# Kernel tuning notes

Measured on AMD Instinct MI355X. Metric: run time of the kernel, lower is better.

The kernel has to match this reference:

```python
import jax, jax.numpy as jnp
import numpy as np

IN_F = 4096
OUT_F = 4096
Q_RANK = 2
R_RANK = 2
SCALE = 1.0
B, S = 2, 2048


def setup_inputs() -> dict:
    key = jax.random.key(0)
    ks = jax.random.split(key, 8)
    inp = jax.random.normal(ks[0], (B, S, IN_F), jnp.float32)
    # Q, R come from a QR decomposition of linear.weight.t(); random stand-ins with
    # matching shapes and O(1) scale are fine for a numerical baseline.
    Q = jax.random.normal(ks[1], (IN_F, OUT_F), jnp.float32) / np.sqrt(IN_F).astype(np.float32)
    R = jax.random.normal(ks[2], (OUT_F, OUT_F), jnp.float32) / np.sqrt(OUT_F).astype(np.float32)
    # kron_Q1/Q2 are initialized to identity in __init__ (never re-initialized);
    # add small noise so the rotation path is non-trivial.
    sq1 = IN_F // Q_RANK
    kron_Q1 = jnp.eye(sq1, dtype=jnp.float32) + 0.01 * jax.random.normal(ks[3], (sq1, sq1), jnp.float32)
    kron_Q2 = jnp.eye(Q_RANK, dtype=jnp.float32) + 0.01 * jax.random.normal(ks[4], (Q_RANK, Q_RANK), jnp.float32)
    # kron_R1/R2 use normal init with std = 1/size.
    sr1 = OUT_F // R_RANK
    kron_R1 = jax.random.normal(ks[5], (sr1, sr1), jnp.float32) / sr1
    kron_R2 = jax.random.normal(ks[6], (R_RANK, R_RANK), jnp.float32) / R_RANK
    # lambda_matrix inits to zeros; use small noise so the delta term is exercised.
    lambda_matrix = 0.01 * jax.random.normal(ks[7], (OUT_F,), jnp.float32)
    return {"input": inp, "Q": Q, "R": R, "kron_Q1": kron_Q1, "kron_Q2": kron_Q2,
            "kron_R1": kron_R1, "kron_R2": kron_R2, "lambda_matrix": lambda_matrix}


def reference(input, Q, R, kron_Q1, kron_Q2, kron_R1, kron_R2, lambda_matrix):
    rotation = jnp.kron(kron_Q1, kron_Q2)          # [in, in]
    orth = jnp.kron(kron_R1, kron_R2)              # [out, out]
    # orth @ diag(lambda) @ orth.T without materializing diag
    R_eff = R + (orth * lambda_matrix[None, :]) @ orth.T  # [out, out]
    W_t = rotation @ (Q @ R_eff)                   # [in, out]
    # F.linear(input, W_t.t()) == input @ W_t; dropout is identity in eval; bias=False
    return (input @ W_t) * SCALE
```

## Files before the change

### kernel.cpp

```cpp
#include <hip/hip_runtime.h>
#include <stdint.h>


typedef unsigned short u16;
typedef short bf16x8 __attribute__((ext_vector_type(8)));
typedef float f32x16 __attribute__((ext_vector_type(16)));

__device__ __forceinline__ u16 f2bf(float f) {
  union { float f; uint32_t u; } v; v.f = f;
  return (u16)((v.u + 0x7FFFu + ((v.u >> 16) & 1u)) >> 16);
}

__device__ __forceinline__ void store_out(float* p, float v) { *p = v; }
__device__ __forceinline__ void store_out(u16* p, float v) { *p = f2bf(v); }

__device__ __forceinline__ void gload_lds16(const u16* g, u16* l) {
  __builtin_amdgcn_global_load_lds(
      (__attribute__((address_space(1))) void*)(uintptr_t)g,
      (__attribute__((address_space(3))) void*)l, 16, 0, 0);
}

#define MFMA32(a, b, c) __builtin_amdgcn_mfma_f32_32x32x16_bf16((a), (b), (c), 0, 0, 0)

template <typename OutT>
__global__ __launch_bounds__(512, 2) void gemm256(
    const u16* __restrict__ A, const u16* __restrict__ Bt, OutT* __restrict__ C,
    int M, int N, int K, int ldC, long long sA, long long sC) {
  extern __shared__ __align__(16) u16 smem[];
  u16* ldsA = smem;
  u16* ldsB = smem + 32768;

  const int tid  = (int)threadIdx.x;
  const int lane = tid & 63;
  const int wid  = tid >> 6;
  const int wr   = wid >> 2;
  const int wc   = wid & 3;

  const int tilesX = (int)gridDim.x;
  const int tilesXY = tilesX * (int)gridDim.y;
  const int nwg = tilesXY * (int)gridDim.z;
  const int bid = ((int)blockIdx.z * (int)gridDim.y + (int)blockIdx.y) * tilesX + (int)blockIdx.x;
  const int swz = (bid & 7) * (nwg >> 3) + (bid >> 3);
  const int z   = swz / tilesXY;
  const int rem = swz % tilesXY;
  const int brow = (rem / tilesX) << 8;
  const int bcol = (rem % tilesX) << 8;
  A += (size_t)z * sA;
  C += (size_t)z * sC;

  const int hh  = (lane & 15) >> 1;
  const int gq  = lane >> 4;
  const int par = lane & 1;
  const int sfr = (((gq + 4 * par) ^ hh) << 3) + (hh << 6);
  const int abase = wr * 4096 + sfr;
  const int bbase = (wc >> 1) * 4096 + (wc & 1) * 2048 + sfr;

  {
  }
  const int Rw  = (wid << 3) + (lane >> 3);
  const int hS  = Rw & 7;
  const int xS  = (lane & 7) ^ hS;
  const int srow = ((Rw >> 4) << 5) + ((xS & 1) << 4) + (hS << 1) + (xS >> 2);
  const int scol = (((Rw >> 3) & 1) << 4) + (((xS >> 1) & 1) << 3);
  const size_t gA0 = (size_t)(brow + srow) * K + scol;
  const size_t gB0 = (size_t)(bcol + srow) * K + scol;
  const size_t rstep = (size_t)K << 7;
  const int sdst = wid * 512;

  const int NC = K >> 5;

  f32x16 acc[4][2] = {};
  bf16x8 af[2][2], bf[2][2];

#define STG_A(c, rh) gload_lds16(A + gA0 + (rh) * rstep + (size_t)(c) * 32, \
    ldsA + ((c) & 3) * 8192 + (rh) * 4096 + sdst)
#define STG_B(c, rh) gload_lds16(Bt + gB0 + (rh) * rstep + (size_t)(c) * 32, \
    ldsB + ((c) & 3) * 8192 + (rh) * 4096 + sdst)
#define VM8 asm volatile("s_waitcnt vmcnt(8)" ::: "memory")
#define VM4 asm volatile("s_waitcnt vmcnt(4)" ::: "memory")
#define VM0 asm volatile("s_waitcnt vmcnt(0)" ::: "memory")
#define NOPW (void)0

#define P_EVEN(bb, S, W) do {                                                   \
    const u16* _pa = ldsA + (bb) * 8192 + abase;                                \
    const u16* _pb = ldsB + (bb) * 8192 + bbase;                                \
    af[0][0] = *(const bf16x8*)(_pa);                                           \
    af[0][1] = *(const bf16x8*)(_pa + 512);                                     \
    af[1][0] = *(const bf16x8*)(_pa + 1024);                                    \
    af[1][1] = *(const bf16x8*)(_pa + 1536);                                    \
    bf[0][0] = *(const bf16x8*)(_pb);                                           \
    bf[0][1] = *(const bf16x8*)(_pb + 512);                                     \
    bf[1][0] = *(const bf16x8*)(_pb + 1024);                                    \
    bf[1][1] = *(const bf16x8*)(_pb + 1536);                                    \
    S;                                                                          \
    __builtin_amdgcn_s_barrier();                                               \
    __builtin_amdgcn_s_setprio(1);                                              \
    acc[0][0] = MFMA32(af[0][0], bf[0][0], acc[0][0]);                          \
    acc[0][0] = MFMA32(af[0][1], bf[0][1], acc[0][0]);                          \
    acc[0][1] = MFMA32(af[0][0], bf[1][0], acc[0][1]);                          \
    acc[0][1] = MFMA32(af[0][1], bf[1][1], acc[0][1]);                          \
    acc[1][0] = MFMA32(af[1][0], bf[0][0], acc[1][0]);                          \
    acc[1][0] = MFMA32(af[1][1], bf[0][1], acc[1][0]);                          \
    acc[1][1] = MFMA32(af[1][0], bf[1][0], acc[1][1]);                          \
    acc[1][1] = MFMA32(af[1][1], bf[1][1], acc[1][1]);                          \
    __builtin_amdgcn_s_setprio(0);                                              \
    W;                                                                          \
    __builtin_amdgcn_s_barrier();                                               \
  } while (0)

#define P_ODD(bb, S, W) do {                                                    \
    const u16* _pa = ldsA + (bb) * 8192 + abase;                                \
    af[0][0] = *(const bf16x8*)(_pa + 2048);                                    \
    af[0][1] = *(const bf16x8*)(_pa + 2560);                                    \
    af[1][0] = *(const bf16x8*)(_pa + 3072);                                    \
    af[1][1] = *(const bf16x8*)(_pa + 3584);                                    \
    S;                                                                          \
    __builtin_amdgcn_s_barrier();                                               \
    __builtin_amdgcn_s_setprio(1);                                              \
    acc[2][0] = MFMA32(af[0][0], bf[0][0], acc[2][0]);                          \
    acc[2][0] = MFMA32(af[0][1], bf[0][1], acc[2][0]);                          \
    acc[2][1] = MFMA32(af[0][0], bf[1][0], acc[2][1]);                          \
    acc[2][1] = MFMA32(af[0][1], bf[1][1], acc[2][1]);                          \
    acc[3][0] = MFMA32(af[1][0], bf[0][0], acc[3][0]);                          \
    acc[3][0] = MFMA32(af[1][1], bf[0][1], acc[3][0]);                          \
    acc[3][1] = MFMA32(af[1][0], bf[1][0], acc[3][1]);                          \
    acc[3][1] = MFMA32(af[1][1], bf[1][1], acc[3][1]);                          \
    __builtin_amdgcn_s_setprio(0);                                              \
    W;                                                                          \
    __builtin_amdgcn_s_barrier();                                               \
  } while (0)

#define ITER(bb, c, DO3, DO4, W1, W3) do {                                      \
    P_EVEN((bb),     if (DO3) { STG_A((c) + 3, 0); STG_A((c) + 3, 1); }, NOPW); \
    P_ODD ((bb),     if (DO3) { STG_B((c) + 3, 0); STG_B((c) + 3, 1); }, W1);   \
    P_EVEN((bb) + 1, if (DO4) { STG_A((c) + 4, 0); STG_A((c) + 4, 1); }, NOPW); \
    P_ODD ((bb) + 1, if (DO4) { STG_B((c) + 4, 0); STG_B((c) + 4, 1); }, W3);   \
  } while (0)

  STG_A(0, 0); STG_A(0, 1); STG_B(0, 0); STG_B(0, 1);
  STG_A(1, 0); STG_A(1, 1); STG_B(1, 0); STG_B(1, 1);
  STG_A(2, 0); STG_A(2, 1); STG_B(2, 0); STG_B(2, 1);
  VM8;
  __builtin_amdgcn_s_barrier();

  for (int c = 0; c + 4 < NC; c += 4) {
    ITER(0, c,     1, 1, VM8, VM8);
    ITER(2, c + 2, 1, 1, VM8, VM8);
  }
  ITER(0, NC - 4, 1, 0, VM8, VM4);
  ITER(2, NC - 2, 0, 0, VM0, NOPW);

#undef ITER
#undef P_EVEN
#undef P_ODD
#undef STG_A
#undef STG_B
#undef VM8
#undef VM4
#undef VM0
#undef NOPW

  const int l31 = lane & 31;
  const int lg2 = lane >> 5;
#pragma unroll
  for (int m = 0; m < 4; ++m) {
    const int rb = brow + wr * 128 + m * 32 + 4 * lg2;
#pragma unroll
    for (int n = 0; n < 2; ++n) {
      const int cc = bcol + wc * 64 + n * 32 + l31;
#pragma unroll
      for (int q = 0; q < 4; ++q)
#pragma unroll
        for (int j = 0; j < 4; ++j)
          store_out(&C[(size_t)(rb + 8 * q + j) * ldC + cc], acc[m][n][q * 4 + j]);
    }
  }
}

__global__ void trans_kernel(const float* __restrict__ in, u16* __restrict__ out, int n) {
  __shared__ float t[32][33];
  const int bx = (int)blockIdx.x * 32, by = (int)blockIdx.y * 32;
  const int x = (int)threadIdx.x, y0 = (int)threadIdx.y;
#pragma unroll
  for (int dy = 0; dy < 32; dy += 8)
    t[y0 + dy][x] = in[(size_t)(bx + y0 + dy) * n + by + x];
  __syncthreads();
#pragma unroll
  for (int dy = 0; dy < 32; dy += 8)
    out[(size_t)(by + y0 + dy) * n + bx + x] = f2bf(t[x][y0 + dy]);
}

__global__ void transperm_kernel(const float* __restrict__ in, u16* __restrict__ out) {
  __shared__ float t[32][33];
  const int bx = (int)blockIdx.x * 32, by = (int)blockIdx.y * 32;
  const int x = (int)threadIdx.x, y0 = (int)threadIdx.y;
#pragma unroll
  for (int dy = 0; dy < 32; dy += 8)
    t[y0 + dy][x] = in[(size_t)(bx + y0 + dy) * 4096 + by + x];
  __syncthreads();
  const int r = bx + x;
  const int cp = ((r & 1) << 11) | (r >> 1);
#pragma unroll
  for (int dy = 0; dy < 32; dy += 8)
    out[(size_t)(by + y0 + dy) * 4096 + cp] = f2bf(t[x][y0 + dy]);
}

__global__ void transadd_kernel(const float* __restrict__ R, const float* __restrict__ Dsub,
                                u16* __restrict__ out) {
  __shared__ float t[32][33];
  const int bx = (int)blockIdx.x * 32, by = (int)blockIdx.y * 32;
  const int x = (int)threadIdx.x, y0 = (int)threadIdx.y;
#pragma unroll
  for (int dy = 0; dy < 32; dy += 8)
    t[y0 + dy][x] = R[(size_t)(bx + y0 + dy) * 4096 + by + x];
  __syncthreads();
  const int j = bx + x;
#pragma unroll
  for (int dy = 0; dy < 32; dy += 8) {
    const int i = by + y0 + dy;
    const int s = ((i & 1) << 1) | (j & 1);
    const float d = Dsub[(size_t)s * 4194304 + ((size_t)(i >> 1) << 11) + (j >> 1)];
    out[(size_t)i * 4096 + j] = f2bf(t[x][y0 + dy] + d);
  }
}

__global__ void scale_r1_kernel(const float* __restrict__ R1, const float* __restrict__ R2,
                                const float* __restrict__ lam,
                                u16* __restrict__ R1bf, u16* __restrict__ Asc) {
  const int idx = (int)blockIdx.x * 256 + (int)threadIdx.x;
  const int i1 = idx >> 9, k1 = (idx & 511) << 2;
  const float4 r1 = *(const float4*)(R1 + (size_t)i1 * 2048 + k1);
  const float4 l0 = *(const float4*)(lam + 2 * k1);
  const float4 l1 = *(const float4*)(lam + 2 * k1 + 4);
  const float le[4] = {l0.x, l0.z, l1.x, l1.z};
  const float lo[4] = {l0.y, l0.w, l1.y, l1.w};
  const float rv[4] = {r1.x, r1.y, r1.z, r1.w};
  ushort4 rb;
  rb.x = f2bf(r1.x); rb.y = f2bf(r1.y); rb.z = f2bf(r1.z); rb.w = f2bf(r1.w);
  *(ushort4*)(R1bf + (size_t)i1 * 2048 + k1) = rb;
#pragma unroll
  for (int s = 0; s < 4; ++s) {
    const int i2 = s >> 1, j2 = s & 1;
    const float c0 = R2[i2 * 2] * R2[j2 * 2];
    const float c1 = R2[i2 * 2 + 1] * R2[j2 * 2 + 1];
    ushort4 o;
    u16* dst = Asc + (size_t)s * 4194304 + (size_t)i1 * 2048 + k1;
    o.x = f2bf(rv[0] * (le[0] * c0 + lo[0] * c1));
    o.y = f2bf(rv[1] * (le[1] * c0 + lo[1] * c1));
    o.z = f2bf(rv[2] * (le[2] * c0 + lo[2] * c1));
    o.w = f2bf(rv[3] * (le[3] * c0 + lo[3] * c1));
    *(ushort4*)dst = o;
  }
}

__global__ void tprep_kernel(const float* __restrict__ in, const float* __restrict__ Q2,
                             u16* __restrict__ T) {
  const int idx = (int)blockIdx.x * 256 + (int)threadIdx.x;
  const int s = idx >> 9, k1 = (idx & 511) << 2;
  const float4 a = *(const float4*)(in + (size_t)s * 4096 + 2 * k1);
  const float4 b = *(const float4*)(in + (size_t)s * 4096 + 2 * k1 + 4);
  const float e[4] = {a.x, a.z, b.x, b.z};
  const float o[4] = {a.y, a.w, b.y, b.w};
  const float q00 = Q2[0], q01 = Q2[1], q10 = Q2[2], q11 = Q2[3];
  ushort4 t0, t1;
  t0.x = f2bf(e[0] * q00 + o[0] * q10); t1.x = f2bf(e[0] * q01 + o[0] * q11);
  t0.y = f2bf(e[1] * q00 + o[1] * q10); t1.y = f2bf(e[1] * q01 + o[1] * q11);
  t0.z = f2bf(e[2] * q00 + o[2] * q10); t1.z = f2bf(e[2] * q01 + o[2] * q11);
  t0.w = f2bf(e[3] * q00 + o[3] * q10); t1.w = f2bf(e[3] * q01 + o[3] * q11);
  *(ushort4*)(T + (size_t)s * 2048 + k1) = t0;
  *(ushort4*)(T + 8388608 + (size_t)s * 2048 + k1) = t1;
}

extern "C" void kernel_launch(void* const* d_in, const int* in_sizes, int n_in,
                              void* d_out, int out_size, void* d_ws, size_t ws_size,
                              hipStream_t stream) {
  const float* input = (const float*)d_in[0];
  const float* Q     = (const float*)d_in[1];
  const float* R     = (const float*)d_in[2];
  const float* Q1    = (const float*)d_in[3];
  const float* Q2    = (const float*)d_in[4];
  const float* R1    = (const float*)d_in[5];
  const float* R2    = (const float*)d_in[6];
  const float* lam   = (const float*)d_in[7];
  float* out = (float*)d_out;

  const size_t MB = 1024ull * 1024ull;
  char* ws = (char*)d_ws;
  u16* R1bf  = (u16*)(ws + 0 * MB);
  u16* Asc   = (u16*)(ws + 8 * MB);
  u16* Q1tb  = (u16*)(ws + 40 * MB);
  u16* T     = (u16*)(ws + 48 * MB);
  u16* Qtp   = (u16*)(ws + 80 * MB);
  u16* rteff = (u16*)(ws + 112 * MB);
  u16* X1p   = (u16*)(ws + 144 * MB);
  u16* X2    = Asc;
  float* Dsub = (float*)d_out;

  {
    void (*pf)(const u16*, const u16*, float*, int, int, int, int, long long, long long) = gemm256<float>;
    void (*pb)(const u16*, const u16*, u16*, int, int, int, int, long long, long long)   = gemm256<u16>;
    (void)hipFuncSetAttribute((const void*)pf, hipFuncAttributeMaxDynamicSharedMemorySize, 131072);
    (void)hipFuncSetAttribute((const void*)pb, hipFuncAttributeMaxDynamicSharedMemorySize, 131072);
  }

  const dim3 tb(32, 8);
  trans_kernel<<<dim3(64, 64), tb, 0, stream>>>(Q1, Q1tb, 2048);
  transperm_kernel<<<dim3(128, 128), tb, 0, stream>>>(Q, Qtp);
  scale_r1_kernel<<<4096, 256, 0, stream>>>(R1, R2, lam, R1bf, Asc);
  tprep_kernel<<<8192, 256, 0, stream>>>(input, Q2, T);
  gemm256<float><<<dim3(8, 8, 4), 512, 131072, stream>>>(
      Asc, R1bf, Dsub, 2048, 2048, 2048, 2048, 4194304LL, 4194304LL);
  transadd_kernel<<<dim3(128, 128), tb, 0, stream>>>(R, Dsub, rteff);
  gemm256<u16><<<dim3(8, 16, 2), 512, 131072, stream>>>(
      T, Q1tb, X1p, 4096, 2048, 2048, 4096, 8388608LL, 2048LL);
  gemm256<u16><<<dim3(16, 16, 1), 512, 131072, stream>>>(
      X1p, Qtp, X2, 4096, 4096, 4096, 4096, 0LL, 0LL);
  gemm256<float><<<dim3(16, 16, 1), 512, 131072, stream>>>(
      X2, rteff, out, 4096, 4096, 4096, 4096, 0LL, 0LL);
}
```

Baseline: 507.5 us.

## Merge even/odd half-phases into one phase per K-chunk with full-stage prefetch

Replaces the two half-phases per K-chunk (A rows 0-1, then rows 2-3, each with its own barrier pair) with a single phase. Each phase loads all four A fragments plus the B fragments, issues 16 MFMAs, and prefetches a whole stage (A and B) three chunks ahead. This halves the number of barriers and waitcnt points per chunk and gives longer MFMA runs between synchronisations. In exchange it needs more VGPRs for the extra A fragments, which may lower occupancy. It also reworks the vmcnt accounting, and the tail of the loop has to drain the prefetched stages correctly.

Result: slower. 549.2 us (+8.2%).

```diff
diff --git a/kernel.cpp b/kernel.cpp
--- a/kernel.cpp
+++ b/kernel.cpp
@@ -55,8 +55,6 @@
   const int abase = wr * 4096 + sfr;
   const int bbase = (wc >> 1) * 4096 + (wc & 1) * 2048 + sfr;
 
-  {
-  }
   const int Rw  = (wid << 3) + (lane >> 3);
   const int hS  = Rw & 7;
   const int xS  = (lane & 7) ^ hS;
@@ -70,28 +68,34 @@
   const int NC = K >> 5;
 
   f32x16 acc[4][2] = {};
-  bf16x8 af[2][2], bf[2][2];
+  bf16x8 af[4][2], bf[2][2];
 
 #define STG_A(c, rh) gload_lds16(A + gA0 + (rh) * rstep + (size_t)(c) * 32, \
     ldsA + ((c) & 3) * 8192 + (rh) * 4096 + sdst)
 #define STG_B(c, rh) gload_lds16(Bt + gB0 + (rh) * rstep + (size_t)(c) * 32, \
     ldsB + ((c) & 3) * 8192 + (rh) * 4096 + sdst)
+#define STAGE(c) do { STG_A(c, 0); STG_A(c, 1); STG_B(c, 0); STG_B(c, 1); } while (0)
 #define VM8 asm volatile("s_waitcnt vmcnt(8)" ::: "memory")
 #define VM4 asm volatile("s_waitcnt vmcnt(4)" ::: "memory")
 #define VM0 asm volatile("s_waitcnt vmcnt(0)" ::: "memory")
 #define NOPW (void)0
 
-#define P_EVEN(bb, S, W) do {                                                   \
+#define PH(bb, S, W) do {                                                       \
+    __builtin_amdgcn_sched_barrier(0);                                          \
     const u16* _pa = ldsA + (bb) * 8192 + abase;                                \
     const u16* _pb = ldsB + (bb) * 8192 + bbase;                                \
+    bf[0][0] = *(const bf16x8*)(_pb);                                           \
+    bf[0][1] = *(const bf16x8*)(_pb + 512);                                     \
+    bf[1][0] = *(const bf16x8*)(_pb + 1024);                                    \
+    bf[1][1] = *(const bf16x8*)(_pb + 1536);                                    \
     af[0][0] = *(const bf16x8*)(_pa);                                           \
     af[0][1] = *(const bf16x8*)(_pa + 512);                                     \
     af[1][0] = *(const bf16x8*)(_pa + 1024);                                    \
     af[1][1] = *(const bf16x8*)(_pa + 1536);                                    \
-    bf[0][0] = *(const bf16x8*)(_pb);                                           \
-    bf[0][1] = *(const bf16x8*)(_pb + 512);                                     \
-    bf[1][0] = *(const bf16x8*)(_pb + 1024);                                    \
-    bf[1][1] = *(const bf16x8*)(_pb + 1536);                                    \
+    af[2][0] = *(const bf16x8*)(_pa + 2048);                                    \
+    af[2][1] = *(const bf16x8*)(_pa + 2560);                                    \
+    af[3][0] = *(const bf16x8*)(_pa + 3072);                                    \
+    af[3][1] = *(const bf16x8*)(_pa + 3584);                                    \
     S;                                                                          \
     __builtin_amdgcn_s_barrier();                                               \
     __builtin_amdgcn_s_setprio(1);                                              \
@@ -103,56 +107,36 @@
     acc[1][0] = MFMA32(af[1][1], bf[0][1], acc[1][0]);                          \
     acc[1][1] = MFMA32(af[1][0], bf[1][0], acc[1][1]);                          \
     acc[1][1] = MFMA32(af[1][1], bf[1][1], acc[1][1]);                          \
+    acc[2][0] = MFMA32(af[2][0], bf[0][0], acc[2][0]);                          \
+    acc[2][0] = MFMA32(af[2][1], bf[0][1], acc[2][0]);                          \
+    acc[2][1] = MFMA32(af[2][0], bf[1][0], acc[2][1]);                          \
+    acc[2][1] = MFMA32(af[2][1], bf[1][1], acc[2][1]);                          \
+    acc[3][0] = MFMA32(af[3][0], bf[0][0], acc[3][0]);                          \
+    acc[3][0] = MFMA32(af[3][1], bf[0][1], acc[3][0]);                          \
+    acc[3][1] = MFMA32(af[3][0], bf[1][0], acc[3][1]);                          \
+    acc[3][1] = MFMA32(af[3][1], bf[1][1], acc[3][1]);                          \
     __builtin_amdgcn_s_setprio(0);                                              \
     W;                                                                          \
     __builtin_amdgcn_s_barrier();                                               \
   } while (0)
 
-#define P_ODD(bb, S, W) do {                                                    \
-    const u16* _pa = ldsA + (bb) * 8192 + abase;                                \
-    af[0][0] = *(const bf16x8*)(_pa + 2048);                                    \
-    af[0][1] = *(const bf16x8*)(_pa + 2560);                                    \
-    af[1][0] = *(const bf16x8*)(_pa + 3072);                                    \
-    af[1][1] = *(const bf16x8*)(_pa + 3584);                                    \
-    S;                                                                          \
-    __builtin_amdgcn_s_barrier();                                               \
-    __builtin_amdgcn_s_setprio(1);                                              \
-    acc[2][0] = MFMA32(af[0][0], bf[0][0], acc[2][0]);                          \
-    acc[2][0] = MFMA32(af[0][1], bf[0][1], acc[2][0]);                          \
-    acc[2][1] = MFMA32(af[0][0], bf[1][0], acc[2][1]);                          \
-    acc[2][1] = MFMA32(af[0][1], bf[1][1], acc[2][1]);                          \
-    acc[3][0] = MFMA32(af[1][0], bf[0][0], acc[3][0]);                          \
-    acc[3][0] = MFMA32(af[1][1], bf[0][1], acc[3][0]);                          \
-    acc[3][1] = MFMA32(af[1][0], bf[1][0], acc[3][1]);                          \
-    acc[3][1] = MFMA32(af[1][1], bf[1][1], acc[3][1]);                          \
-    __builtin_amdgcn_s_setprio(0);                                              \
-    W;                                                                          \
-    __builtin_amdgcn_s_barrier();                                               \
-  } while (0)
-
-#define ITER(bb, c, DO3, DO4, W1, W3) do {                                      \
-    P_EVEN((bb),     if (DO3) { STG_A((c) + 3, 0); STG_A((c) + 3, 1); }, NOPW); \
-    P_ODD ((bb),     if (DO3) { STG_B((c) + 3, 0); STG_B((c) + 3, 1); }, W1);   \
-    P_EVEN((bb) + 1, if (DO4) { STG_A((c) + 4, 0); STG_A((c) + 4, 1); }, NOPW); \
-    P_ODD ((bb) + 1, if (DO4) { STG_B((c) + 4, 0); STG_B((c) + 4, 1); }, W3);   \
-  } while (0)
-
-  STG_A(0, 0); STG_A(0, 1); STG_B(0, 0); STG_B(0, 1);
-  STG_A(1, 0); STG_A(1, 1); STG_B(1, 0); STG_B(1, 1);
-  STG_A(2, 0); STG_A(2, 1); STG_B(2, 0); STG_B(2, 1);
+  STAGE(0); STAGE(1); STAGE(2);
   VM8;
   __builtin_amdgcn_s_barrier();
 
   for (int c = 0; c + 4 < NC; c += 4) {
-    ITER(0, c,     1, 1, VM8, VM8);
-    ITER(2, c + 2, 1, 1, VM8, VM8);
-  }
-  ITER(0, NC - 4, 1, 0, VM8, VM4);
-  ITER(2, NC - 2, 0, 0, VM0, NOPW);
-
-#undef ITER
-#undef P_EVEN
-#undef P_ODD
+    PH(0, STAGE(c + 3), VM8);
+    PH(1, STAGE(c + 4), VM8);
+    PH(2, STAGE(c + 5), VM8);
+    PH(3, STAGE(c + 6), VM8);
+  }
+  PH(0, STAGE(NC - 1), VM8);
+  PH(1, NOPW, VM4);
+  PH(2, NOPW, VM0);
+  PH(3, NOPW, NOPW);
+
+#undef PH
+#undef STAGE
 #undef STG_A
 #undef STG_B
 #undef VM8
```
